# Kernel tuning notes

Measured on AMD Instinct MI355X. Metric: run time of the kernel, lower is better.

## Reference

```python
import jax, jax.numpy as jnp
import numpy as np

N_NODES = 20000
N_EDGES = 5000
STEPS = 50
INFECTION_RATE = 0.01
RECOVERY_RATE = 0.038
EDGE_DENSITY = 0.002  # ~10 hyperedges per node on average


def setup_inputs() -> dict:
    key = jax.random.key(0)
    k1, k2 = jax.random.split(key, 2)
    # initial SIR state per node: valid probability rows summing to 1
    u = jax.random.uniform(k1, (N_NODES, 3), dtype=jnp.float32)
    x = u / u.sum(axis=1, keepdims=True)
    # binary hypergraph incidence matrix (num_hyperedges, num_nodes)
    H = (jax.random.uniform(k2, (N_EDGES, N_NODES)) < EDGE_DENSITY).astype(jnp.float32)
    beta = jnp.full((N_NODES,), INFECTION_RATE, dtype=jnp.float32)
    gamma = jnp.full((N_NODES,), RECOVERY_RATE, dtype=jnp.float32)
    return {"x": x, "H": H, "beta": beta, "gamma": gamma, "steps": STEPS}


def reference(x, H, beta, gamma, steps):
    # x: (N, 3) [S, I, R] per node; H: (E, N) incidence.
    def step(state, _):
        S, I, R = state[:, 0], state[:, 1], state[:, 2]
        # hypergraph message passing: node -> hyperedge -> node
        new_cases = beta * (S * (H.T @ (H @ I)))
        new_recovery = gamma * I
        nxt = jnp.stack(
            [S - new_cases, I + new_cases - new_recovery, R + new_recovery], axis=1
        )
        nxt = jnp.maximum(nxt, 0.0)                       # clamp(min=0)
        nxt = nxt / nxt.sum(axis=1, keepdims=True)        # per-node row normalize
        return nxt, nxt

    _, traj = jax.lax.scan(step, x, None, length=steps - 1)
    # output[0] = initial state, then steps-1 simulated updates -> (steps, N, 3)
    return jnp.concatenate([x[None], traj], axis=0)
```

## Files before the change

### kernel.cpp

```cpp
#include <hip/hip_runtime.h>


#define EDGE_CAP 96
#define NODE_CAP 32
#define NIDX_REG 16
#define COOP_BLOCKS 256
#define COOP_THREADS 512
#define BAR_LINES 8
#define BAR_STRIDE 128
#define BAR_UINTS (BAR_LINES * BAR_STRIDE)

__global__ void zero_counts_kernel(int* edge_cnt, int* node_cnt, unsigned* bar,
                                   int n_edges, int n_nodes) {
    int i = blockIdx.x * blockDim.x + threadIdx.x;
    if (i < BAR_UINTS) bar[i] = 0u;
    if (i < n_edges) edge_cnt[i] = 0;
    if (i < n_nodes) node_cnt[i] = 0;
}

__global__ void build_adjacency_kernel(const float* __restrict__ H,
                                       int* __restrict__ edge_cnt,
                                       int* __restrict__ edge_nodes,
                                       int* __restrict__ node_cnt,
                                       int* __restrict__ node_edges,
                                       int n_nodes) {
    __shared__ int cnt;
    __shared__ int cols[EDGE_CAP];
    const int e = blockIdx.x;
    if (threadIdx.x == 0) cnt = 0;
    __syncthreads();
    const uint4* row4 = (const uint4*)(H + (size_t)e * n_nodes);
    const int n4 = n_nodes >> 2;
    for (int c4 = threadIdx.x; c4 < n4; c4 += blockDim.x) {
        uint4 v = row4[c4];
        if ((v.x | v.y | v.z | v.w) != 0u) {
            int cbase = c4 << 2;
            if (v.x) { int p = atomicAdd(&cnt, 1); if (p < EDGE_CAP) cols[p] = cbase; }
            if (v.y) { int p = atomicAdd(&cnt, 1); if (p < EDGE_CAP) cols[p] = cbase + 1; }
            if (v.z) { int p = atomicAdd(&cnt, 1); if (p < EDGE_CAP) cols[p] = cbase + 2; }
            if (v.w) { int p = atomicAdd(&cnt, 1); if (p < EDGE_CAP) cols[p] = cbase + 3; }
        }
    }
    if (threadIdx.x == 0) {
        const float* row = H + (size_t)e * n_nodes;
        for (int c = n4 << 2; c < n_nodes; ++c)
            if (row[c] != 0.0f) { int p = atomicAdd(&cnt, 1); if (p < EDGE_CAP) cols[p] = c; }
    }
    __syncthreads();
    int cn = min(cnt, EDGE_CAP);
    if (threadIdx.x == 0) edge_cnt[e] = cn;
    for (int i = threadIdx.x; i < cn; i += blockDim.x) {
        int c = cols[i];
        edge_nodes[e * EDGE_CAP + i] = c;
        int q = atomicAdd(&node_cnt[c], 1);
        if (q < NODE_CAP) node_edges[c * NODE_CAP + q] = e;
    }
}

__device__ __forceinline__ float coh_load(const float* p) {
    return __hip_atomic_load(p, __ATOMIC_RELAXED, __HIP_MEMORY_SCOPE_AGENT);
}
__device__ __forceinline__ void coh_storef(float* p, float v) {
    __hip_atomic_store(p, v, __ATOMIC_RELAXED, __HIP_MEMORY_SCOPE_AGENT);
}

__device__ __forceinline__ void bar_arrive(unsigned* bar) {
    asm volatile("s_waitcnt vmcnt(0)" ::: "memory");
    __syncthreads();
    if (threadIdx.x == 0)
        __hip_atomic_fetch_add(&bar[(blockIdx.x & (BAR_LINES - 1)) * BAR_STRIDE], 1u,
                               __ATOMIC_RELAXED, __HIP_MEMORY_SCOPE_AGENT);
}
__device__ __forceinline__ void bar_wait(unsigned* bar, unsigned target) {
    if (threadIdx.x == 0) {
        for (;;) {
            unsigned sum = 0;
            #pragma unroll
            for (int i = 0; i < BAR_LINES; ++i)
                sum += __hip_atomic_load(&bar[i * BAR_STRIDE], __ATOMIC_RELAXED,
                                         __HIP_MEMORY_SCOPE_AGENT);
            if (sum >= target) break;
            __builtin_amdgcn_s_sleep(1);
        }
    }
    __syncthreads();
    asm volatile("" ::: "memory");
}

__global__ __launch_bounds__(COOP_THREADS) void sir_steps_kernel(
        const float* __restrict__ x,
        const int* __restrict__ edge_cnt, const int* __restrict__ edge_nodes,
        const int* __restrict__ node_cnt, const int* __restrict__ node_edges,
        const float* __restrict__ beta, const float* __restrict__ gamma,
        float* __restrict__ y, float* __restrict__ I,
        float* __restrict__ out,
        int n_nodes, int n_edges, int steps, unsigned* bar) {
    const int b  = blockIdx.x;
    const int tx = threadIdx.x;

    const int node_chunk = (n_nodes + gridDim.x - 1) / gridDim.x;
    const int edge_chunk = (n_edges + gridDim.x - 1) / gridDim.x;
    const int n = b * node_chunk + tx;
    const bool own = (tx < node_chunk) && (n < n_nodes);

    const int k = tx >> 4, gl = tx & 15;
    const int e = b * edge_chunk + k;
    const bool has_edge = (k < edge_chunk) && (e < n_edges);

    int ecnt = 0;
    const int* en = edge_nodes;
    if (has_edge) { ecnt = min(edge_cnt[e], EDGE_CAP); en = edge_nodes + e * EDGE_CAP; }
    int eidx[6];
    #pragma unroll
    for (int i = 0; i < 6; ++i) {
        int j = i * 16 + gl;
        eidx[i] = (has_edge && j < ecnt) ? en[j] : n_nodes;
    }

    int ncnt = 0;
    const int* ne = node_edges;
    float bet = 0.0f, gam = 0.0f;
    if (own) { ncnt = min(node_cnt[n], NODE_CAP); ne = node_edges + n * NODE_CAP;
               bet = beta[n]; gam = gamma[n]; }
    int nidx[NIDX_REG];
    #pragma unroll
    for (int i = 0; i < NIDX_REG; ++i)
        nidx[i] = (own && i < ncnt) ? ne[i] : n_edges;

    float s = 0.0f, iv = 0.0f, r = 0.0f;
    if (own) {
        s = x[n * 3 + 0]; iv = x[n * 3 + 1]; r = x[n * 3 + 2];
        coh_storef(&I[n], iv);
        out[n * 3 + 0] = s; out[n * 3 + 1] = iv; out[n * 3 + 2] = r;
    }
    if (b == 0 && tx == 0) { coh_storef(&I[n_nodes], 0.0f); coh_storef(&y[n_edges], 0.0f); }
    unsigned bars = 0;
    bar_arrive(bar); bars += gridDim.x; bar_wait(bar, bars);

    for (int t = 1; t < steps; ++t) {
        if (has_edge) {
            float a0 = coh_load(&I[eidx[0]]);
            float a1 = coh_load(&I[eidx[1]]);
            float a2 = coh_load(&I[eidx[2]]);
            float a3 = coh_load(&I[eidx[3]]);
            float a4 = coh_load(&I[eidx[4]]);
            float a5 = coh_load(&I[eidx[5]]);
            float acc = a0 + a1 + a2 + a3 + a4 + a5;
            acc += __shfl_down(acc, 8, 16);
            acc += __shfl_down(acc, 4, 16);
            acc += __shfl_down(acc, 2, 16);
            acc += __shfl_down(acc, 1, 16);
            if (gl == 0) coh_storef(&y[e], acc);
        }
        bar_arrive(bar); bars += gridDim.x; bar_wait(bar, bars);

        if (own) {
            float tv[NIDX_REG];
            #pragma unroll
            for (int i = 0; i < NIDX_REG; ++i) tv[i] = coh_load(&y[nidx[i]]);
            float z = 0.0f;
            #pragma unroll
            for (int i = 0; i < NIDX_REG; ++i) z += tv[i];
            for (int i = NIDX_REG; i < ncnt; ++i) z += coh_load(&y[ne[i]]);
            float nc = bet * s * z;
            float nr = gam * iv;
            float s2 = fmaxf(s - nc, 0.0f);
            float i2 = fmaxf(iv + nc - nr, 0.0f);
            float r2 = fmaxf(r + nr, 0.0f);
            float inv = 1.0f / (s2 + i2 + r2);
            s = s2 * inv; iv = i2 * inv; r = r2 * inv;
            coh_storef(&I[n], iv);
        }
        bar_arrive(bar); bars += gridDim.x;
        if (own) {
            float* ot = out + (size_t)t * n_nodes * 3 + (size_t)n * 3;
            ot[0] = s; ot[1] = iv; ot[2] = r;
        }
        if (t + 1 < steps) bar_wait(bar, bars);
    }
}

extern "C" void kernel_launch(void* const* d_in, const int* in_sizes, int n_in,
                              void* d_out, int out_size, void* d_ws, size_t ws_size,
                              hipStream_t stream) {
    const float* x     = (const float*)d_in[0];
    const float* H     = (const float*)d_in[1];
    const float* beta  = (const float*)d_in[2];
    const float* gamma = (const float*)d_in[3];
    float* out = (float*)d_out;

    const int n_nodes = in_sizes[0] / 3;
    const int n_edges = in_sizes[1] / n_nodes;
    const int steps   = out_size / in_sizes[0];

    char* ws = (char*)d_ws;
    unsigned* bar     = (unsigned*)ws;                    ws += (size_t)BAR_UINTS * 4;
    int*   edge_cnt   = (int*)ws;                         ws += (size_t)n_edges * 4;
    int*   node_cnt   = (int*)ws;                         ws += (size_t)n_nodes * 4;
    int*   edge_nodes = (int*)ws;                         ws += (size_t)n_edges * EDGE_CAP * 4;
    int*   node_edges = (int*)ws;                         ws += (size_t)n_nodes * NODE_CAP * 4;
    float* y          = (float*)ws;                       ws += ((size_t)n_edges + 1) * 4;
    float* I          = (float*)ws;                       ws += ((size_t)n_nodes + 1) * 4;

    {
        int mx = max(n_edges, max(n_nodes, (int)BAR_UINTS));
        zero_counts_kernel<<<(mx + 255) / 256, 256, 0, stream>>>(edge_cnt, node_cnt, bar,
                                                                 n_edges, n_nodes);
    }
    build_adjacency_kernel<<<n_edges, 256, 0, stream>>>(H, edge_cnt, edge_nodes,
                                                        node_cnt, node_edges, n_nodes);
    sir_steps_kernel<<<COOP_BLOCKS, COOP_THREADS, 0, stream>>>(
        x, edge_cnt, edge_nodes, node_cnt, node_edges, beta, gamma,
        y, I, out, n_nodes, n_edges, steps, bar);
}
```

Baseline: 1.011 ms.

## Replace counter grid barrier with per-block phase flags and ballot-based H scan

The grid barrier now has each block store its phase number to its own flag, and one wavefront polls all 128 flags in parallel with a ballot. This replaces the atomic-add counters spread over 8 cache lines. The persistent kernel drops to 128 blocks of 1024 threads so there are fewer participants per barrier. The adjacency build now scans H in two passes: a ballot records which float4 chunks are nonzero, then only those chunks are reloaded. The aim is to cut barrier latency across about 100 phases and to reduce divergent work in the dense H scan. In exchange, each block now has twice as many threads, which may hurt occupancy or per-thread register budget, and the flag scheme is hard-wired to 128 blocks.

```diff
diff --git a/kernel.cpp b/kernel.cpp
--- a/kernel.cpp
+++ b/kernel.cpp
@@ -4,16 +4,16 @@
 #define EDGE_CAP 96
 #define NODE_CAP 32
 #define NIDX_REG 16
-#define COOP_BLOCKS 256
-#define COOP_THREADS 512
-#define BAR_LINES 8
-#define BAR_STRIDE 128
-#define BAR_UINTS (BAR_LINES * BAR_STRIDE)
-
-__global__ void zero_counts_kernel(int* edge_cnt, int* node_cnt, unsigned* bar,
+#define COOP_BLOCKS 128
+#define COOP_THREADS 1024
+#define NFLAGS 128
+
+typedef unsigned int uint4_ev __attribute__((ext_vector_type(4)));
+
+__global__ void zero_counts_kernel(int* edge_cnt, int* node_cnt, unsigned* flags,
                                    int n_edges, int n_nodes) {
     int i = blockIdx.x * blockDim.x + threadIdx.x;
-    if (i < BAR_UINTS) bar[i] = 0u;
+    if (i < NFLAGS) flags[i] = 0u;
     if (i < n_edges) edge_cnt[i] = 0;
     if (i < n_nodes) node_cnt[i] = 0;
 }
@@ -26,30 +26,48 @@
                                        int n_nodes) {
     __shared__ int cnt;
     __shared__ int cols[EDGE_CAP];
-    const int e = blockIdx.x;
-    if (threadIdx.x == 0) cnt = 0;
-    __syncthreads();
-    const uint4* row4 = (const uint4*)(H + (size_t)e * n_nodes);
+    __shared__ unsigned long long qmask[128];
+    const int e  = blockIdx.x;
+    const int tx = threadIdx.x;
+    if (tx == 0) cnt = 0;
+    const float* row = H + (size_t)e * n_nodes;
+    const uint4_ev* row4 = (const uint4_ev*)row;
     const int n4 = n_nodes >> 2;
-    for (int c4 = threadIdx.x; c4 < n4; c4 += blockDim.x) {
-        uint4 v = row4[c4];
-        if ((v.x | v.y | v.z | v.w) != 0u) {
-            int cbase = c4 << 2;
+    const int niter = (n4 + 255) >> 8;
+
+    for (int i = 0; i < niter; ++i) {
+        int q = (i << 8) + tx;
+        uint4_ev v = {0u, 0u, 0u, 0u};
+        if (q < n4) v = row4[q];
+        unsigned long long m = __ballot((v.x | v.y | v.z | v.w) != 0u);
+        if ((tx & 63) == 0) qmask[(i << 2) + (tx >> 6)] = m;
+    }
+    __syncthreads();
+
+    const int nslots = niter << 2;
+    for (int sIdx = tx; sIdx < nslots; sIdx += blockDim.x) {
+        unsigned long long m = qmask[sIdx];
+        int qbase = ((sIdx >> 2) << 8) + ((sIdx & 3) << 6);
+        while (m) {
+            int lane = __builtin_ctzll(m); m &= m - 1;
+            int q = qbase + lane;
+            uint4_ev v = row4[q];
+            int cbase = q << 2;
             if (v.x) { int p = atomicAdd(&cnt, 1); if (p < EDGE_CAP) cols[p] = cbase; }
             if (v.y) { int p = atomicAdd(&cnt, 1); if (p < EDGE_CAP) cols[p] = cbase + 1; }
             if (v.z) { int p = atomicAdd(&cnt, 1); if (p < EDGE_CAP) cols[p] = cbase + 2; }
             if (v.w) { int p = atomicAdd(&cnt, 1); if (p < EDGE_CAP) cols[p] = cbase + 3; }
         }
     }
-    if (threadIdx.x == 0) {
-        const float* row = H + (size_t)e * n_nodes;
+    if (tx == 0) {
         for (int c = n4 << 2; c < n_nodes; ++c)
             if (row[c] != 0.0f) { int p = atomicAdd(&cnt, 1); if (p < EDGE_CAP) cols[p] = c; }
     }
     __syncthreads();
+
     int cn = min(cnt, EDGE_CAP);
-    if (threadIdx.x == 0) edge_cnt[e] = cn;
-    for (int i = threadIdx.x; i < cn; i += blockDim.x) {
+    if (tx == 0) edge_cnt[e] = cn;
+    for (int i = tx; i < cn; i += blockDim.x) {
         int c = cols[i];
         edge_nodes[e * EDGE_CAP + i] = c;
         int q = atomicAdd(&node_cnt[c], 1);
@@ -63,23 +81,24 @@
 __device__ __forceinline__ void coh_storef(float* p, float v) {
     __hip_atomic_store(p, v, __ATOMIC_RELAXED, __HIP_MEMORY_SCOPE_AGENT);
 }
-
-__device__ __forceinline__ void bar_arrive(unsigned* bar) {
+__device__ __forceinline__ unsigned coh_loadu(const unsigned* p) {
+    return __hip_atomic_load(p, __ATOMIC_RELAXED, __HIP_MEMORY_SCOPE_AGENT);
+}
+__device__ __forceinline__ void coh_storeu(unsigned* p, unsigned v) {
+    __hip_atomic_store(p, v, __ATOMIC_RELAXED, __HIP_MEMORY_SCOPE_AGENT);
+}
+
+__device__ __forceinline__ void bar_pub(unsigned* flags, unsigned ph) {
     asm volatile("s_waitcnt vmcnt(0)" ::: "memory");
     __syncthreads();
-    if (threadIdx.x == 0)
-        __hip_atomic_fetch_add(&bar[(blockIdx.x & (BAR_LINES - 1)) * BAR_STRIDE], 1u,
-                               __ATOMIC_RELAXED, __HIP_MEMORY_SCOPE_AGENT);
-}
-__device__ __forceinline__ void bar_wait(unsigned* bar, unsigned target) {
-    if (threadIdx.x == 0) {
+    if (threadIdx.x == 0) coh_storeu(&flags[blockIdx.x], ph);
+}
+__device__ __forceinline__ void bar_poll(unsigned* flags, unsigned ph) {
+    if (threadIdx.x < 64) {
         for (;;) {
-            unsigned sum = 0;
-            #pragma unroll
-            for (int i = 0; i < BAR_LINES; ++i)
-                sum += __hip_atomic_load(&bar[i * BAR_STRIDE], __ATOMIC_RELAXED,
-                                         __HIP_MEMORY_SCOPE_AGENT);
-            if (sum >= target) break;
+            unsigned a = coh_loadu(&flags[threadIdx.x]);
+            unsigned b = coh_loadu(&flags[64 + threadIdx.x]);
+            if (__ballot((a < ph) || (b < ph)) == 0ull) break;
             __builtin_amdgcn_s_sleep(1);
         }
     }
@@ -94,7 +113,7 @@
         const float* __restrict__ beta, const float* __restrict__ gamma,
         float* __restrict__ y, float* __restrict__ I,
         float* __restrict__ out,
-        int n_nodes, int n_edges, int steps, unsigned* bar) {
+        int n_nodes, int n_edges, int steps, unsigned* flags) {
     const int b  = blockIdx.x;
     const int tx = threadIdx.x;
 
@@ -134,8 +153,8 @@
         out[n * 3 + 0] = s; out[n * 3 + 1] = iv; out[n * 3 + 2] = r;
     }
     if (b == 0 && tx == 0) { coh_storef(&I[n_nodes], 0.0f); coh_storef(&y[n_edges], 0.0f); }
-    unsigned bars = 0;
-    bar_arrive(bar); bars += gridDim.x; bar_wait(bar, bars);
+    unsigned ph = 1;
+    bar_pub(flags, ph); bar_poll(flags, ph);
 
     for (int t = 1; t < steps; ++t) {
         if (has_edge) {
@@ -152,7 +171,7 @@
             acc += __shfl_down(acc, 1, 16);
             if (gl == 0) coh_storef(&y[e], acc);
         }
-        bar_arrive(bar); bars += gridDim.x; bar_wait(bar, bars);
+        ++ph; bar_pub(flags, ph); bar_poll(flags, ph);
 
         if (own) {
             float tv[NIDX_REG];
@@ -171,12 +190,12 @@
             s = s2 * inv; iv = i2 * inv; r = r2 * inv;
             coh_storef(&I[n], iv);
         }
-        bar_arrive(bar); bars += gridDim.x;
+        ++ph; bar_pub(flags, ph);
         if (own) {
             float* ot = out + (size_t)t * n_nodes * 3 + (size_t)n * 3;
             ot[0] = s; ot[1] = iv; ot[2] = r;
         }
-        if (t + 1 < steps) bar_wait(bar, bars);
+        if (t + 1 < steps) bar_poll(flags, ph);
     }
 }
 
@@ -194,7 +213,7 @@
     const int steps   = out_size / in_sizes[0];
 
     char* ws = (char*)d_ws;
-    unsigned* bar     = (unsigned*)ws;                    ws += (size_t)BAR_UINTS * 4;
+    unsigned* flags   = (unsigned*)ws;                    ws += (size_t)NFLAGS * 4;
     int*   edge_cnt   = (int*)ws;                         ws += (size_t)n_edges * 4;
     int*   node_cnt   = (int*)ws;                         ws += (size_t)n_nodes * 4;
     int*   edge_nodes = (int*)ws;                         ws += (size_t)n_edges * EDGE_CAP * 4;
@@ -203,13 +222,13 @@
     float* I          = (float*)ws;                       ws += ((size_t)n_nodes + 1) * 4;
 
     {
-        int mx = max(n_edges, max(n_nodes, (int)BAR_UINTS));
-        zero_counts_kernel<<<(mx + 255) / 256, 256, 0, stream>>>(edge_cnt, node_cnt, bar,
+        int mx = max(n_edges, max(n_nodes, (int)NFLAGS));
+        zero_counts_kernel<<<(mx + 255) / 256, 256, 0, stream>>>(edge_cnt, node_cnt, flags,
                                                                  n_edges, n_nodes);
     }
     build_adjacency_kernel<<<n_edges, 256, 0, stream>>>(H, edge_cnt, edge_nodes,
                                                         node_cnt, node_edges, n_nodes);
     sir_steps_kernel<<<COOP_BLOCKS, COOP_THREADS, 0, stream>>>(
         x, edge_cnt, edge_nodes, node_cnt, node_edges, beta, gamma,
-        y, I, out, n_nodes, n_edges, steps, bar);
-}
+        y, I, out, n_nodes, n_edges, steps, flags);
+}
```

New measurement: 1.100 ms. 1.09x slower.

## Replace edge gather phase with fixed-point atomic scatter, triple-buffered per-edge sums

Applied to the files above, without the earlier changes.

The per-step edge-gather phase and its grid barrier are removed. Each node now scatters its quantized infection value into per-edge integer accumulators using atomics, and three rotating buffers let the next step accumulate and a spare buffer be zeroed within a single barrier per step. The adjacency build first ballots nonzero vector chunks, then revisits only those chunks. The grid changes to 128 blocks of 1024 threads. Fixed-point quantization at 2^24 adds rounding error, and contended atomics on padded slots replace plain loads.

```diff
diff --git a/kernel.cpp b/kernel.cpp
--- a/kernel.cpp
+++ b/kernel.cpp
@@ -4,18 +4,24 @@
 #define EDGE_CAP 96
 #define NODE_CAP 32
 #define NIDX_REG 16
-#define COOP_BLOCKS 256
-#define COOP_THREADS 512
+#define COOP_BLOCKS 128
+#define COOP_THREADS 1024
 #define BAR_LINES 8
 #define BAR_STRIDE 128
 #define BAR_UINTS (BAR_LINES * BAR_STRIDE)
-
-__global__ void zero_counts_kernel(int* edge_cnt, int* node_cnt, unsigned* bar,
-                                   int n_edges, int n_nodes) {
+#define YPAD 16
+#define ISCALE 16777216.0f
+#define INV_ISCALE 5.9604644775390625e-8f
+
+typedef unsigned int uint4_ev __attribute__((ext_vector_type(4)));
+
+__global__ void zero_ws_kernel(int* edge_cnt, int* node_cnt, unsigned* bar,
+                               int* ybufs, int n_edges, int n_nodes, int ytot) {
     int i = blockIdx.x * blockDim.x + threadIdx.x;
     if (i < BAR_UINTS) bar[i] = 0u;
     if (i < n_edges) edge_cnt[i] = 0;
     if (i < n_nodes) node_cnt[i] = 0;
+    if (i < ytot) ybufs[i] = 0;
 }
 
 __global__ void build_adjacency_kernel(const float* __restrict__ H,
@@ -26,30 +32,48 @@
                                        int n_nodes) {
     __shared__ int cnt;
     __shared__ int cols[EDGE_CAP];
-    const int e = blockIdx.x;
-    if (threadIdx.x == 0) cnt = 0;
-    __syncthreads();
-    const uint4* row4 = (const uint4*)(H + (size_t)e * n_nodes);
+    __shared__ unsigned long long qmask[128];
+    const int e  = blockIdx.x;
+    const int tx = threadIdx.x;
+    if (tx == 0) cnt = 0;
+    const float* row = H + (size_t)e * n_nodes;
+    const uint4_ev* row4 = (const uint4_ev*)row;
     const int n4 = n_nodes >> 2;
-    for (int c4 = threadIdx.x; c4 < n4; c4 += blockDim.x) {
-        uint4 v = row4[c4];
-        if ((v.x | v.y | v.z | v.w) != 0u) {
-            int cbase = c4 << 2;
+    const int niter = (n4 + 255) >> 8;
+
+    for (int i = 0; i < niter; ++i) {
+        int q = (i << 8) + tx;
+        uint4_ev v = {0u, 0u, 0u, 0u};
+        if (q < n4) v = row4[q];
+        unsigned long long m = __ballot((v.x | v.y | v.z | v.w) != 0u);
+        if ((tx & 63) == 0) qmask[(i << 2) + (tx >> 6)] = m;
+    }
+    __syncthreads();
+
+    const int nslots = niter << 2;
+    for (int sIdx = tx; sIdx < nslots; sIdx += blockDim.x) {
+        unsigned long long m = qmask[sIdx];
+        int qbase = ((sIdx >> 2) << 8) + ((sIdx & 3) << 6);
+        while (m) {
+            int lane = __builtin_ctzll(m); m &= m - 1;
+            int q = qbase + lane;
+            uint4_ev v = row4[q];
+            int cbase = q << 2;
             if (v.x) { int p = atomicAdd(&cnt, 1); if (p < EDGE_CAP) cols[p] = cbase; }
             if (v.y) { int p = atomicAdd(&cnt, 1); if (p < EDGE_CAP) cols[p] = cbase + 1; }
             if (v.z) { int p = atomicAdd(&cnt, 1); if (p < EDGE_CAP) cols[p] = cbase + 2; }
             if (v.w) { int p = atomicAdd(&cnt, 1); if (p < EDGE_CAP) cols[p] = cbase + 3; }
         }
     }
-    if (threadIdx.x == 0) {
-        const float* row = H + (size_t)e * n_nodes;
+    if (tx == 0) {
         for (int c = n4 << 2; c < n_nodes; ++c)
             if (row[c] != 0.0f) { int p = atomicAdd(&cnt, 1); if (p < EDGE_CAP) cols[p] = c; }
     }
     __syncthreads();
+
     int cn = min(cnt, EDGE_CAP);
-    if (threadIdx.x == 0) edge_cnt[e] = cn;
-    for (int i = threadIdx.x; i < cn; i += blockDim.x) {
+    if (tx == 0) edge_cnt[e] = cn;
+    for (int i = tx; i < cn; i += blockDim.x) {
         int c = cols[i];
         edge_nodes[e * EDGE_CAP + i] = c;
         int q = atomicAdd(&node_cnt[c], 1);
@@ -57,10 +81,10 @@
     }
 }
 
-__device__ __forceinline__ float coh_load(const float* p) {
+__device__ __forceinline__ int coh_loadi(const int* p) {
     return __hip_atomic_load(p, __ATOMIC_RELAXED, __HIP_MEMORY_SCOPE_AGENT);
 }
-__device__ __forceinline__ void coh_storef(float* p, float v) {
+__device__ __forceinline__ void coh_storei(int* p, int v) {
     __hip_atomic_store(p, v, __ATOMIC_RELAXED, __HIP_MEMORY_SCOPE_AGENT);
 }
 
@@ -89,10 +113,9 @@
 
 __global__ __launch_bounds__(COOP_THREADS) void sir_steps_kernel(
         const float* __restrict__ x,
-        const int* __restrict__ edge_cnt, const int* __restrict__ edge_nodes,
         const int* __restrict__ node_cnt, const int* __restrict__ node_edges,
         const float* __restrict__ beta, const float* __restrict__ gamma,
-        float* __restrict__ y, float* __restrict__ I,
+        int* __restrict__ yb0, int* __restrict__ yb1, int* __restrict__ yb2,
         float* __restrict__ out,
         int n_nodes, int n_edges, int steps, unsigned* bar) {
     const int b  = blockIdx.x;
@@ -102,20 +125,6 @@
     const int edge_chunk = (n_edges + gridDim.x - 1) / gridDim.x;
     const int n = b * node_chunk + tx;
     const bool own = (tx < node_chunk) && (n < n_nodes);
-
-    const int k = tx >> 4, gl = tx & 15;
-    const int e = b * edge_chunk + k;
-    const bool has_edge = (k < edge_chunk) && (e < n_edges);
-
-    int ecnt = 0;
-    const int* en = edge_nodes;
-    if (has_edge) { ecnt = min(edge_cnt[e], EDGE_CAP); en = edge_nodes + e * EDGE_CAP; }
-    int eidx[6];
-    #pragma unroll
-    for (int i = 0; i < 6; ++i) {
-        int j = i * 16 + gl;
-        eidx[i] = (has_edge && j < ecnt) ? en[j] : n_nodes;
-    }
 
     int ncnt = 0;
     const int* ne = node_edges;
@@ -130,38 +139,28 @@
     float s = 0.0f, iv = 0.0f, r = 0.0f;
     if (own) {
         s = x[n * 3 + 0]; iv = x[n * 3 + 1]; r = x[n * 3 + 2];
-        coh_storef(&I[n], iv);
         out[n * 3 + 0] = s; out[n * 3 + 1] = iv; out[n * 3 + 2] = r;
-    }
-    if (b == 0 && tx == 0) { coh_storef(&I[n_nodes], 0.0f); coh_storef(&y[n_edges], 0.0f); }
+        int ivq = (int)rintf(iv * ISCALE);
+        #pragma unroll
+        for (int i = 0; i < NIDX_REG; ++i)
+            if (i < ncnt) atomicAdd(&yb1[nidx[i] * YPAD], ivq);
+        for (int i = NIDX_REG; i < ncnt; ++i) atomicAdd(&yb1[ne[i] * YPAD], ivq);
+    }
     unsigned bars = 0;
     bar_arrive(bar); bars += gridDim.x; bar_wait(bar, bars);
 
+    int* cur = yb1; int* nxt = yb2; int* zer = yb0;
     for (int t = 1; t < steps; ++t) {
-        if (has_edge) {
-            float a0 = coh_load(&I[eidx[0]]);
-            float a1 = coh_load(&I[eidx[1]]);
-            float a2 = coh_load(&I[eidx[2]]);
-            float a3 = coh_load(&I[eidx[3]]);
-            float a4 = coh_load(&I[eidx[4]]);
-            float a5 = coh_load(&I[eidx[5]]);
-            float acc = a0 + a1 + a2 + a3 + a4 + a5;
-            acc += __shfl_down(acc, 8, 16);
-            acc += __shfl_down(acc, 4, 16);
-            acc += __shfl_down(acc, 2, 16);
-            acc += __shfl_down(acc, 1, 16);
-            if (gl == 0) coh_storef(&y[e], acc);
-        }
-        bar_arrive(bar); bars += gridDim.x; bar_wait(bar, bars);
-
         if (own) {
-            float tv[NIDX_REG];
+            int tvq[NIDX_REG];
             #pragma unroll
-            for (int i = 0; i < NIDX_REG; ++i) tv[i] = coh_load(&y[nidx[i]]);
+            for (int i = 0; i < NIDX_REG; ++i) tvq[i] = coh_loadi(&cur[nidx[i] * YPAD]);
             float z = 0.0f;
             #pragma unroll
-            for (int i = 0; i < NIDX_REG; ++i) z += tv[i];
-            for (int i = NIDX_REG; i < ncnt; ++i) z += coh_load(&y[ne[i]]);
+            for (int i = 0; i < NIDX_REG; ++i) z += (float)tvq[i];
+            for (int i = NIDX_REG; i < ncnt; ++i)
+                z += (float)coh_loadi(&cur[ne[i] * YPAD]);
+            z *= INV_ISCALE;
             float nc = bet * s * z;
             float nr = gam * iv;
             float s2 = fmaxf(s - nc, 0.0f);
@@ -169,7 +168,20 @@
             float r2 = fmaxf(r + nr, 0.0f);
             float inv = 1.0f / (s2 + i2 + r2);
             s = s2 * inv; iv = i2 * inv; r = r2 * inv;
-            coh_storef(&I[n], iv);
+            if (t + 1 < steps) {
+                int ivq = (int)rintf(iv * ISCALE);
+                #pragma unroll
+                for (int i = 0; i < NIDX_REG; ++i)
+                    if (i < ncnt) atomicAdd(&nxt[nidx[i] * YPAD], ivq);
+                for (int i = NIDX_REG; i < ncnt; ++i) atomicAdd(&nxt[ne[i] * YPAD], ivq);
+            }
+        }
+        if (t + 2 < steps) {
+            int base = b * edge_chunk;
+            for (int zz = tx; zz < edge_chunk; zz += blockDim.x) {
+                int ei = base + zz;
+                if (ei < n_edges) coh_storei(&zer[ei * YPAD], 0);
+            }
         }
         bar_arrive(bar); bars += gridDim.x;
         if (own) {
@@ -177,6 +189,7 @@
             ot[0] = s; ot[1] = iv; ot[2] = r;
         }
         if (t + 1 < steps) bar_wait(bar, bars);
+        int* tmp = cur; cur = nxt; nxt = zer; zer = tmp;
     }
 }
 
@@ -193,23 +206,28 @@
     const int n_edges = in_sizes[1] / n_nodes;
     const int steps   = out_size / in_sizes[0];
 
+    const int yslots = (n_edges + 1) * YPAD;
+    const int ytot   = 3 * yslots;
+
     char* ws = (char*)d_ws;
     unsigned* bar     = (unsigned*)ws;                    ws += (size_t)BAR_UINTS * 4;
     int*   edge_cnt   = (int*)ws;                         ws += (size_t)n_edges * 4;
     int*   node_cnt   = (int*)ws;                         ws += (size_t)n_nodes * 4;
     int*   edge_nodes = (int*)ws;                         ws += (size_t)n_edges * EDGE_CAP * 4;
     int*   node_edges = (int*)ws;                         ws += (size_t)n_nodes * NODE_CAP * 4;
-    float* y          = (float*)ws;                       ws += ((size_t)n_edges + 1) * 4;
-    float* I          = (float*)ws;                       ws += ((size_t)n_nodes + 1) * 4;
+    int*   ybufs      = (int*)ws;                         ws += (size_t)ytot * 4;
+    int*   yb0 = ybufs;
+    int*   yb1 = ybufs + yslots;
+    int*   yb2 = ybufs + 2 * yslots;
 
     {
-        int mx = max(n_edges, max(n_nodes, (int)BAR_UINTS));
-        zero_counts_kernel<<<(mx + 255) / 256, 256, 0, stream>>>(edge_cnt, node_cnt, bar,
-                                                                 n_edges, n_nodes);
+        int mx = max(ytot, max(n_edges, max(n_nodes, (int)BAR_UINTS)));
+        zero_ws_kernel<<<(mx + 255) / 256, 256, 0, stream>>>(edge_cnt, node_cnt, bar,
+                                                             ybufs, n_edges, n_nodes, ytot);
     }
     build_adjacency_kernel<<<n_edges, 256, 0, stream>>>(H, edge_cnt, edge_nodes,
                                                         node_cnt, node_edges, n_nodes);
     sir_steps_kernel<<<COOP_BLOCKS, COOP_THREADS, 0, stream>>>(
-        x, edge_cnt, edge_nodes, node_cnt, node_edges, beta, gamma,
-        y, I, out, n_nodes, n_edges, steps, bar);
-}
+        x, node_cnt, node_edges, beta, gamma,
+        yb0, yb1, yb2, out, n_nodes, n_edges, steps, bar);
+}
```

After: 1.263 ms. 1.25x slower.

## Fuse adjacency build into persistent SIR kernel with ballot-based sparse row scan

Applied to the files above, without the earlier changes.

Merges the adjacency-building kernel into the persistent simulation kernel, so each of 256 blocks scans a slice of H rows before a grid barrier and then runs the time steps. The row scan first prefetches uint4 chunks and records nonzero masks with a wavefront ballot, then re-reads only the nonzero chunks to append column indices. Block size doubles to 1024 threads. This removes a kernel launch and the per-edge launch overhead, at the cost of one extra grid barrier and only 256 blocks streaming the 400MB H matrix, which may limit memory-level parallelism.

```diff
diff --git a/kernel.cpp b/kernel.cpp
--- a/kernel.cpp
+++ b/kernel.cpp
@@ -4,60 +4,23 @@
 #define EDGE_CAP 96
 #define NODE_CAP 32
 #define NIDX_REG 16
-#define COOP_BLOCKS 256
-#define COOP_THREADS 512
+#define BLOCKS 256
+#define THREADS 1024
 #define BAR_LINES 8
 #define BAR_STRIDE 128
 #define BAR_UINTS (BAR_LINES * BAR_STRIDE)
 
-__global__ void zero_counts_kernel(int* edge_cnt, int* node_cnt, unsigned* bar,
-                                   int n_edges, int n_nodes) {
+typedef unsigned int uint4_ev __attribute__((ext_vector_type(4)));
+
+__global__ void zero_ws_kernel(int* edge_cnt, int* node_cnt, unsigned* bar,
+                               int n_edges, int n_nodes) {
     int i = blockIdx.x * blockDim.x + threadIdx.x;
     if (i < BAR_UINTS) bar[i] = 0u;
     if (i < n_edges) edge_cnt[i] = 0;
     if (i < n_nodes) node_cnt[i] = 0;
 }
 
-__global__ void build_adjacency_kernel(const float* __restrict__ H,
-                                       int* __restrict__ edge_cnt,
-                                       int* __restrict__ edge_nodes,
-                                       int* __restrict__ node_cnt,
-                                       int* __restrict__ node_edges,
-                                       int n_nodes) {
-    __shared__ int cnt;
-    __shared__ int cols[EDGE_CAP];
-    const int e = blockIdx.x;
-    if (threadIdx.x == 0) cnt = 0;
-    __syncthreads();
-    const uint4* row4 = (const uint4*)(H + (size_t)e * n_nodes);
-    const int n4 = n_nodes >> 2;
-    for (int c4 = threadIdx.x; c4 < n4; c4 += blockDim.x) {
-        uint4 v = row4[c4];
-        if ((v.x | v.y | v.z | v.w) != 0u) {
-            int cbase = c4 << 2;
-            if (v.x) { int p = atomicAdd(&cnt, 1); if (p < EDGE_CAP) cols[p] = cbase; }
-            if (v.y) { int p = atomicAdd(&cnt, 1); if (p < EDGE_CAP) cols[p] = cbase + 1; }
-            if (v.z) { int p = atomicAdd(&cnt, 1); if (p < EDGE_CAP) cols[p] = cbase + 2; }
-            if (v.w) { int p = atomicAdd(&cnt, 1); if (p < EDGE_CAP) cols[p] = cbase + 3; }
-        }
-    }
-    if (threadIdx.x == 0) {
-        const float* row = H + (size_t)e * n_nodes;
-        for (int c = n4 << 2; c < n_nodes; ++c)
-            if (row[c] != 0.0f) { int p = atomicAdd(&cnt, 1); if (p < EDGE_CAP) cols[p] = c; }
-    }
-    __syncthreads();
-    int cn = min(cnt, EDGE_CAP);
-    if (threadIdx.x == 0) edge_cnt[e] = cn;
-    for (int i = threadIdx.x; i < cn; i += blockDim.x) {
-        int c = cols[i];
-        edge_nodes[e * EDGE_CAP + i] = c;
-        int q = atomicAdd(&node_cnt[c], 1);
-        if (q < NODE_CAP) node_edges[c * NODE_CAP + q] = e;
-    }
-}
-
-__device__ __forceinline__ float coh_load(const float* p) {
+__device__ __forceinline__ float coh_loadf(const float* p) {
     return __hip_atomic_load(p, __ATOMIC_RELAXED, __HIP_MEMORY_SCOPE_AGENT);
 }
 __device__ __forceinline__ void coh_storef(float* p, float v) {
@@ -87,16 +50,78 @@
     asm volatile("" ::: "memory");
 }
 
-__global__ __launch_bounds__(COOP_THREADS) void sir_steps_kernel(
-        const float* __restrict__ x,
-        const int* __restrict__ edge_cnt, const int* __restrict__ edge_nodes,
-        const int* __restrict__ node_cnt, const int* __restrict__ node_edges,
+__global__ __launch_bounds__(THREADS) void sir_mega_kernel(
+        const float* __restrict__ x, const float* __restrict__ H,
         const float* __restrict__ beta, const float* __restrict__ gamma,
-        float* __restrict__ y, float* __restrict__ I,
-        float* __restrict__ out,
+        int* __restrict__ edge_cnt, int* __restrict__ edge_nodes,
+        int* __restrict__ node_cnt, int* __restrict__ node_edges,
+        float* __restrict__ y, float* __restrict__ I, float* __restrict__ out,
         int n_nodes, int n_edges, int steps, unsigned* bar) {
     const int b  = blockIdx.x;
     const int tx = threadIdx.x;
+
+    __shared__ int cnt;
+    __shared__ int cols[EDGE_CAP];
+    __shared__ unsigned long long qmask[128];
+
+    const int rpb = (n_edges + gridDim.x - 1) / gridDim.x;
+    const int n4 = n_nodes >> 2;
+    const int niter = (n4 + THREADS - 1) / THREADS;
+    const int e_lo = b * rpb, e_hi = min(e_lo + rpb, n_edges);
+
+    for (int e = e_lo; e < e_hi; ++e) {
+        if (tx == 0) cnt = 0;
+        const uint4_ev* row4 = (const uint4_ev*)(H + (size_t)e * n_nodes);
+
+        uint4_ev vnext = {0u, 0u, 0u, 0u};
+        if (tx < n4) vnext = row4[tx];
+        for (int i = 0; i < niter; ++i) {
+            uint4_ev v = vnext;
+            int qn = (i + 1) * THREADS + tx;
+            vnext = (uint4_ev){0u, 0u, 0u, 0u};
+            if (i + 1 < niter && qn < n4) vnext = row4[qn];
+            unsigned long long m = __ballot((v.x | v.y | v.z | v.w) != 0u);
+            if ((tx & 63) == 0) qmask[i * 16 + (tx >> 6)] = m;
+        }
+        __syncthreads();
+
+        const int nslots = niter * 16;
+        for (int sIdx = tx; sIdx < nslots; sIdx += THREADS) {
+            unsigned long long m = qmask[sIdx];
+            int qbase = (sIdx >> 4) * THREADS + (sIdx & 15) * 64;
+            while (m) {
+                int lane = __builtin_ctzll(m); m &= m - 1;
+                int q = qbase + lane;
+                uint4_ev v = row4[q];
+                int cbase = q << 2;
+                if (v.x) { int p = atomicAdd(&cnt, 1); if (p < EDGE_CAP) cols[p] = cbase; }
+                if (v.y) { int p = atomicAdd(&cnt, 1); if (p < EDGE_CAP) cols[p] = cbase + 1; }
+                if (v.z) { int p = atomicAdd(&cnt, 1); if (p < EDGE_CAP) cols[p] = cbase + 2; }
+                if (v.w) { int p = atomicAdd(&cnt, 1); if (p < EDGE_CAP) cols[p] = cbase + 3; }
+            }
+        }
+        if (tx == 0) {
+            const float* row = H + (size_t)e * n_nodes;
+            for (int c = n4 << 2; c < n_nodes; ++c)
+                if (row[c] != 0.0f) { int p = atomicAdd(&cnt, 1); if (p < EDGE_CAP) cols[p] = c; }
+        }
+        __syncthreads();
+
+        int cn = min(cnt, EDGE_CAP);
+        if (tx == 0) edge_cnt[e] = cn;
+        for (int i = tx; i < cn; i += THREADS) {
+            int c = cols[i];
+            edge_nodes[e * EDGE_CAP + i] = c;
+            int qq = atomicAdd(&node_cnt[c], 1);
+            if (qq < NODE_CAP) node_edges[c * NODE_CAP + qq] = e;
+        }
+        __syncthreads();
+    }
+
+    __builtin_amdgcn_fence(__ATOMIC_RELEASE, "agent");
+    unsigned bars = 0;
+    bar_arrive(bar); bars += gridDim.x; bar_wait(bar, bars);
+    __builtin_amdgcn_fence(__ATOMIC_ACQUIRE, "agent");
 
     const int node_chunk = (n_nodes + gridDim.x - 1) / gridDim.x;
     const int edge_chunk = (n_edges + gridDim.x - 1) / gridDim.x;
@@ -116,7 +141,6 @@
         int j = i * 16 + gl;
         eidx[i] = (has_edge && j < ecnt) ? en[j] : n_nodes;
     }
-
     int ncnt = 0;
     const int* ne = node_edges;
     float bet = 0.0f, gam = 0.0f;
@@ -134,17 +158,16 @@
         out[n * 3 + 0] = s; out[n * 3 + 1] = iv; out[n * 3 + 2] = r;
     }
     if (b == 0 && tx == 0) { coh_storef(&I[n_nodes], 0.0f); coh_storef(&y[n_edges], 0.0f); }
-    unsigned bars = 0;
     bar_arrive(bar); bars += gridDim.x; bar_wait(bar, bars);
 
     for (int t = 1; t < steps; ++t) {
         if (has_edge) {
-            float a0 = coh_load(&I[eidx[0]]);
-            float a1 = coh_load(&I[eidx[1]]);
-            float a2 = coh_load(&I[eidx[2]]);
-            float a3 = coh_load(&I[eidx[3]]);
-            float a4 = coh_load(&I[eidx[4]]);
-            float a5 = coh_load(&I[eidx[5]]);
+            float a0 = coh_loadf(&I[eidx[0]]);
+            float a1 = coh_loadf(&I[eidx[1]]);
+            float a2 = coh_loadf(&I[eidx[2]]);
+            float a3 = coh_loadf(&I[eidx[3]]);
+            float a4 = coh_loadf(&I[eidx[4]]);
+            float a5 = coh_loadf(&I[eidx[5]]);
             float acc = a0 + a1 + a2 + a3 + a4 + a5;
             acc += __shfl_down(acc, 8, 16);
             acc += __shfl_down(acc, 4, 16);
@@ -157,11 +180,12 @@
         if (own) {
             float tv[NIDX_REG];
             #pragma unroll
-            for (int i = 0; i < NIDX_REG; ++i) tv[i] = coh_load(&y[nidx[i]]);
+            for (int i = 0; i < NIDX_REG; ++i) tv[i] = coh_loadf(&y[nidx[i]]);
             float z = 0.0f;
             #pragma unroll
             for (int i = 0; i < NIDX_REG; ++i) z += tv[i];
-            for (int i = NIDX_REG; i < ncnt; ++i) z += coh_load(&y[ne[i]]);
+            for (int i = NIDX_REG; i < ncnt; ++i)
+                z += coh_loadf(&y[ne[i]]);
             float nc = bet * s * z;
             float nr = gam * iv;
             float s2 = fmaxf(s - nc, 0.0f);
@@ -204,12 +228,10 @@
 
     {
         int mx = max(n_edges, max(n_nodes, (int)BAR_UINTS));
-        zero_counts_kernel<<<(mx + 255) / 256, 256, 0, stream>>>(edge_cnt, node_cnt, bar,
-                                                                 n_edges, n_nodes);
-    }
-    build_adjacency_kernel<<<n_edges, 256, 0, stream>>>(H, edge_cnt, edge_nodes,
-                                                        node_cnt, node_edges, n_nodes);
-    sir_steps_kernel<<<COOP_BLOCKS, COOP_THREADS, 0, stream>>>(
-        x, edge_cnt, edge_nodes, node_cnt, node_edges, beta, gamma,
+        zero_ws_kernel<<<(mx + 255) / 256, 256, 0, stream>>>(edge_cnt, node_cnt, bar,
+                                                             n_edges, n_nodes);
+    }
+    sir_mega_kernel<<<BLOCKS, THREADS, 0, stream>>>(
+        x, H, beta, gamma, edge_cnt, edge_nodes, node_cnt, node_edges,
         y, I, out, n_nodes, n_edges, steps, bar);
 }
```

Result: slower. 1.123 ms (+11.0%).
